# Kernel tuning notes

Hardware: AMD Instinct MI355X
Metric: run time of the kernel (lower is better)

The kernel has to match this reference:

```python
import jax, jax.numpy as jnp
import numpy as np
import math

HIDDEN = 1024
HEADS = 16
HEAD = HIDDEN // HEADS
B, N = 2, 2048
NEG_INF = -10000.0


def setup_inputs() -> dict:
    key = jax.random.key(0)
    k1, k2, k3, k4, k5 = jax.random.split(key, 5)
    s = 1.0 / math.sqrt(HIDDEN)
    return {
        "encodings": jax.random.normal(k1, (B, N, HIDDEN), dtype=jnp.float32),
        "attn_w": jax.random.uniform(k2, (3 * HIDDEN, HIDDEN), minval=-s, maxval=s, dtype=jnp.float32),
        "attn_b": jax.random.uniform(k3, (3 * HIDDEN,), minval=-s, maxval=s, dtype=jnp.float32),
        "out_w": jax.random.uniform(k4, (HIDDEN, HIDDEN), minval=-s, maxval=s, dtype=jnp.float32),
        "out_b": jax.random.uniform(k5, (HIDDEN,), minval=-s, maxval=s, dtype=jnp.float32),
    }


def reference(encodings, attn_w, attn_b, out_w, out_b):
    b, n, _ = encodings.shape
    qkv = encodings @ attn_w.T + attn_b                      # [b, n, 3*hidden]
    # 'b n (h l) -> b h n l' with l = 3*head_size
    qkv = qkv.reshape(b, n, HEADS, 3 * HEAD).transpose(0, 2, 1, 3)  # [b, h, n, 3d]
    q, k, v = jnp.split(qkv, 3, axis=-1)                     # each [b, h, n, d]
    # causal mask: key index k attends only if k <= q
    mask = jnp.arange(n)[:, None] <= jnp.arange(n)[None, :]  # [k, q]
    scores = jnp.einsum('bhki,bhqi->bhkq', k, q) / math.sqrt(HEAD)
    scores = jnp.where(mask, scores, NEG_INF)
    probs = jax.nn.softmax(scores, axis=2)                   # softmax over k
    combined = jnp.einsum('bhkq,bhkl->bhql', probs, v)       # [b, h, n, d]
    out = combined.transpose(0, 2, 1, 3).reshape(b, n, HIDDEN)
    return out @ out_w.T + out_b
```

## Files before the change

### kernel.cpp

```cpp
#include <hip/hip_runtime.h>
#include <hip/hip_bf16.h>
#include <stdint.h>

#define HIDDEN 1024
#define NHEADS 16
#define DHEAD  64
#define BATCH  2
#define SEQ    2048
#define MROWS  (BATCH*SEQ)
#define QKVC   (3*HIDDEN)

typedef unsigned short u16;
typedef unsigned int   u32;
typedef __bf16 bf16x8 __attribute__((ext_vector_type(8)));
typedef __bf16 bf16x2 __attribute__((ext_vector_type(2)));
typedef float  f32x4  __attribute__((ext_vector_type(4)));
typedef float  f32x16 __attribute__((ext_vector_type(16)));
typedef short  s16x4  __attribute__((ext_vector_type(4)));
typedef u16    u16x8  __attribute__((ext_vector_type(8)));
typedef u32    u32x2  __attribute__((ext_vector_type(2)));

typedef const __attribute__((address_space(1))) void gvoid_t;
typedef       __attribute__((address_space(3))) void lvoid_t;

__device__ __forceinline__ gvoid_t* to_glob(const void* p){
  return (gvoid_t*)(uintptr_t)p;
}
__device__ __forceinline__ lvoid_t* to_lds(void* p){
  return (lvoid_t*)(uintptr_t)p;
}
__device__ __forceinline__ u32 lds_off(const void* p){
  return (u32)(uintptr_t)p;
}

__device__ __forceinline__ u16 f2bf(float x){
  __bf16 h = (__bf16)x;
  return __builtin_bit_cast(u16, h);
}
__device__ __forceinline__ u32 pk2(float a, float b){
  bf16x2 t = { (__bf16)a, (__bf16)b };
  return __builtin_bit_cast(u32, t);
}

#define MFMA32(a, b, c) __builtin_amdgcn_mfma_f32_32x32x16_bf16(a, b, c, 0, 0, 0)

__global__ __launch_bounds__(256) void k_cvt(const float* __restrict__ in,
                                             u16* __restrict__ out, int n4){
  int i = blockIdx.x * 256 + threadIdx.x;
  if (i >= n4) return;
  const float4 v = reinterpret_cast<const float4*>(in)[i];
  ushort4 o;
  o.x = f2bf(v.x); o.y = f2bf(v.y); o.z = f2bf(v.z); o.w = f2bf(v.w);
  reinterpret_cast<ushort4*>(out)[i] = o;
}

template<int NC, bool BF16OUT>
__global__ __launch_bounds__(256) void k_gemm(const u16* __restrict__ A,
                                              const u16* __restrict__ B,
                                              const float* __restrict__ bias,
                                              void* __restrict__ C){
  constexpr int K = HIDDEN;
  __shared__ u16 As[2][128*32];
  __shared__ u16 Bs[2][128*32];
  const int m0 = blockIdx.x * 128;
  const int n0 = blockIdx.y * 128;
  const int tid = threadIdx.x;
  const int w = tid >> 6, l = tid & 63;
  const int wr = w >> 1, wc = w & 1;

  const f32x4 fz = {0.f, 0.f, 0.f, 0.f};
  f32x4 acc[4][4];
  #pragma unroll
  for (int i = 0; i < 4; ++i)
    #pragma unroll
    for (int j = 0; j < 4; ++j) acc[i][j] = fz;

  const u16* ap = A + (size_t)(m0 + (tid >> 2)) * K + (tid & 3) * 8;
  const u16* bp = B + (size_t)(n0 + (tid >> 2)) * K + (tid & 3) * 8;

  auto stage = [&](int k0, int buf){
    __builtin_amdgcn_global_load_lds(to_glob(ap + k0),        to_lds(&As[buf][w*512]),        16, 0, 0);
    __builtin_amdgcn_global_load_lds(to_glob(ap + 64*K + k0), to_lds(&As[buf][2048 + w*512]), 16, 0, 0);
    __builtin_amdgcn_global_load_lds(to_glob(bp + k0),        to_lds(&Bs[buf][w*512]),        16, 0, 0);
    __builtin_amdgcn_global_load_lds(to_glob(bp + 64*K + k0), to_lds(&Bs[buf][2048 + w*512]), 16, 0, 0);
  };

  stage(0, 0);
  __syncthreads();

  for (int k0 = 0; k0 < K; k0 += 32){
    const int cur = (k0 >> 5) & 1;
    if (k0 + 32 < K) stage(k0 + 32, cur ^ 1);

    bf16x8 af[4], bfr[4];
    #pragma unroll
    for (int mf = 0; mf < 4; ++mf)
      af[mf]  = *(const bf16x8*)&As[cur][(wr*64 + mf*16 + (l & 15))*32 + (l >> 4)*8];
    #pragma unroll
    for (int nf = 0; nf < 4; ++nf)
      bfr[nf] = *(const bf16x8*)&Bs[cur][(wc*64 + nf*16 + (l & 15))*32 + (l >> 4)*8];
    #pragma unroll
    for (int mf = 0; mf < 4; ++mf)
      #pragma unroll
      for (int nf = 0; nf < 4; ++nf)
        acc[mf][nf] = __builtin_amdgcn_mfma_f32_16x16x32_bf16(af[mf], bfr[nf], acc[mf][nf], 0, 0, 0);

    __syncthreads();
  }

  #pragma unroll
  for (int nf = 0; nf < 4; ++nf){
    const int col = n0 + wc*64 + nf*16 + (l & 15);
    const float bv = bias[col];
    #pragma unroll
    for (int mf = 0; mf < 4; ++mf){
      #pragma unroll
      for (int r = 0; r < 4; ++r){
        const int row = m0 + wr*64 + mf*16 + (l >> 4)*4 + r;
        const float v = acc[mf][nf][r] + bv;
        if constexpr (BF16OUT) ((u16*)C)[(size_t)row * NC + col] = f2bf(v);
        else                   ((float*)C)[(size_t)row * NC + col] = v;
      }
    }
  }
}

__global__ __launch_bounds__(256, 4) void k_attn(const u16* __restrict__ qkv,
                                                 u16* __restrict__ aout){
  __shared__ u16 smem[16384];

  const int bh = blockIdx.x;
  const int b  = bh >> 4;
  const int h  = bh & 15;
  const int qt = 31 - blockIdx.y;
  const int tid = threadIdx.x;
  const int l  = tid & 63;
  const int w  = tid >> 6;
  const int hr = w >> 1;
  const int wr = w & 1;
  const int t128 = tid & 127;
  const int lw = t128 >> 6;
  const int U  = qt + 1;
  const int kb = hr ? U : 0;
  const int q0 = qt*64 + wr*32;
  const size_t base = (size_t)b * SEQ * QKVC + (size_t)h * 192;
  const float CEXP = 0.18033688011112042f;

  u16* const Kreg = smem + hr*8192;
  u16* const Vreg = smem + hr*8192 + 4096;

  const int cgK = (t128 & 7) ^ ((t128 >> 3) & 7);
  const u16* const baseK = qkv + base + (size_t)(t128 >> 3) * QKVC + 64 + cgK * 8;
  const int vk = ((t128 >> 5) << 2) | ((t128 >> 1) & 3);
  const int vd = (((t128 >> 3) & 3) << 4) | ((t128 & 1) << 3);
  const u16* const baseV = qkv + base + (size_t)vk * QKVC + 128 + vd;

  auto stage = [&](int u, int cb){
    const u16* pk = baseK + (size_t)u * 32 * QKVC;
    const u16* pv = baseV + (size_t)u * 32 * QKVC;
    #pragma unroll
    for (int t = 0; t < 2; ++t){
      __builtin_amdgcn_global_load_lds(to_glob(pk + t*16*QKVC),
                                       to_lds(&Kreg[cb*2048 + t*1024 + lw*512]), 16, 0, 0);
      __builtin_amdgcn_global_load_lds(to_glob(pv + t*16*QKVC),
                                       to_lds(&Vreg[cb*2048 + t*1024 + lw*512]), 16, 0, 0);
    }
  };

  bf16x8 qf[4];
  {
    const u16* qp = qkv + base + (size_t)(q0 + (l & 31)) * QKVC + (l >> 5) * 8;
    #pragma unroll
    for (int dd = 0; dd < 4; ++dd) qf[dd] = *(const bf16x8*)(qp + dd*16);
  }

  f32x16 o0{}, o1{};
  float m = -1e30f, lsum = 0.f;

  stage(kb, 0);
  __syncthreads();

  const u32 vbase = lds_off(Vreg) + (l & 15)*8 + ((l >> 4) & 1)*128 + (l >> 5)*1024;

  for (int it = 0; it < U; ++it){
    const int cur = it & 1;
    const int u = kb + it;
    if (it + 1 < U) stage(kb + it + 1, cur ^ 1);

    f32x16 a0{};
    const int r0 = l & 31;
    #pragma unroll
    for (int dd = 0; dd < 4; ++dd){
      const int c = dd*2 + (l >> 5);
      const bf16x8 k0 = *(const bf16x8*)&Kreg[cur*2048 + r0*64 + ((c ^ (r0 & 7)))*8];
      a0 = MFMA32(k0, qf[dd], a0);
    }

    if (u*32 + 31 > q0){
      const int qg = q0 + (l & 31);
      #pragma unroll
      for (int r = 0; r < 16; ++r){
        const int kg = u*32 + (r & 3) + 8*(r >> 2) + 4*(l >> 5);
        if (kg > qg) a0[r] = -1e30f;
      }
    }

    float pm = -1e30f;
    #pragma unroll
    for (int r = 0; r < 16; ++r) pm = fmaxf(pm, a0[r]);
    pm = fmaxf(pm, __shfl(pm, l ^ 32));

    s16x4 tr[8];
    {
      const u32 vb = vbase + (cur ? 4096u : 0u);
      #pragma unroll
      for (int kk = 0; kk < 2; ++kk){
        asm volatile("ds_read_b64_tr_b16 %0, %4 offset:0\n\t"
                     "ds_read_b64_tr_b16 %1, %4 offset:512\n\t"
                     "ds_read_b64_tr_b16 %2, %4 offset:256\n\t"
                     "ds_read_b64_tr_b16 %3, %4 offset:768"
                     : "=&v"(tr[kk*4+0]), "=&v"(tr[kk*4+1]),
                       "=&v"(tr[kk*4+2]), "=&v"(tr[kk*4+3])
                     : "v"(vb + kk*2048));
      }
    }

    if (__any(pm > m + 64.f)){
      const float mn = fmaxf(m, pm);
      const float corr = exp2f((m - mn) * CEXP);
      m = mn;
      lsum *= corr;
      #pragma unroll
      for (int r = 0; r < 16; ++r){
        const int row = (r & 3) + 8*(r >> 2) + 4*(l >> 5);
        const float cr = __shfl(corr, row | (l & 32));
        o0[r] *= cr; o1[r] *= cr;
      }
    }
    #pragma unroll
    for (int r = 0; r < 16; ++r){
      const float p = exp2f((a0[r] - m) * CEXP);
      lsum += p;
      a0[r] = p;
    }

    asm volatile("s_waitcnt lgkmcnt(0)" ::: "memory");
    __builtin_amdgcn_sched_barrier(0);
    #pragma unroll
    for (int kk = 0; kk < 2; ++kk){
      const int o = kk * 8;
      const u32 x0 = pk2(a0[o+0], a0[o+1]);
      const u32 x1 = pk2(a0[o+2], a0[o+3]);
      const u32 y0 = pk2(a0[o+4], a0[o+5]);
      const u32 y1 = pk2(a0[o+6], a0[o+7]);
      const u32x2 r0v = __builtin_amdgcn_permlane32_swap(x0, y0, false, false);
      const u32x2 r1v = __builtin_amdgcn_permlane32_swap(x1, y1, false, false);
      union { u32 wd[4]; bf16x8 v; } af;
      af.wd[0] = r0v[0]; af.wd[1] = r1v[0]; af.wd[2] = r0v[1]; af.wd[3] = r1v[1];
      union { s16x4 hh[2]; bf16x8 v; } b0, b1;
      b0.hh[0] = tr[kk*4+0]; b0.hh[1] = tr[kk*4+1];
      b1.hh[0] = tr[kk*4+2]; b1.hh[1] = tr[kk*4+3];
      o0 = MFMA32(af.v, b0.v, o0);
      o1 = MFMA32(af.v, b1.v, o1);
    }

    __syncthreads();
  }

  lsum += __shfl(lsum, l ^ 32);
  float* const Osh  = (float*)smem;
  float2* const MLsh = (float2*)((char*)smem + 16384);

  if (hr == 1){
    #pragma unroll
    for (int r = 0; r < 16; ++r){
      Osh[wr*2048 + l*32 + r]      = o0[r];
      Osh[wr*2048 + l*32 + 16 + r] = o1[r];
    }
    MLsh[wr*64 + l] = float2{m, lsum};
  }
  __syncthreads();

  if (hr == 0){
    const float2 ml1 = MLsh[wr*64 + l];
    const float mm = fmaxf(m, ml1.x);
    const float c0 = exp2f((m - mm) * CEXP);
    const float c1 = exp2f((ml1.x - mm) * CEXP);
    const float lm = lsum*c0 + ml1.y*c1;
    const float a0q = c0 / lm;
    const float a1q = c1 / lm;
    #pragma unroll
    for (int r = 0; r < 16; ++r){
      const int row = (r & 3) + 8*(r >> 2) + 4*(l >> 5);
      const float f0 = __shfl(a0q, row | (l & 32));
      const float f1 = __shfl(a1q, row | (l & 32));
      const int qg = q0 + row;
      u16* op = aout + (size_t)(b*SEQ + qg) * HIDDEN + h*64 + (l & 31);
      op[0]  = f2bf(o0[r]*f0 + Osh[wr*2048 + l*32 + r]*f1);
      op[32] = f2bf(o1[r]*f0 + Osh[wr*2048 + l*32 + 16 + r]*f1);
    }
  }
}

extern "C" void kernel_launch(void* const* d_in, const int* in_sizes, int n_in,
                              void* d_out, int out_size, void* d_ws, size_t ws_size,
                              hipStream_t stream){
  const float* enc    = (const float*)d_in[0];
  const float* attn_w = (const float*)d_in[1];
  const float* attn_b = (const float*)d_in[2];
  const float* out_w  = (const float*)d_in[3];
  const float* out_b  = (const float*)d_in[4];

  char* ws = (char*)d_ws;
  u16* enc_bf = (u16*)(ws);
  u16* wa_bf  = (u16*)(ws + (size_t)( 8u << 20));
  u16* wo_bf  = (u16*)(ws + (size_t)(14u << 20));
  u16* qkv    = (u16*)(ws + (size_t)(16u << 20));
  u16* aout   = enc_bf;

  k_cvt<<<dim3((MROWS*HIDDEN/4 + 255)/256), 256, 0, stream>>>(enc,    enc_bf, MROWS*HIDDEN/4);
  k_cvt<<<dim3((QKVC*HIDDEN/4  + 255)/256), 256, 0, stream>>>(attn_w, wa_bf,  QKVC*HIDDEN/4);
  k_cvt<<<dim3((HIDDEN*HIDDEN/4+ 255)/256), 256, 0, stream>>>(out_w,  wo_bf,  HIDDEN*HIDDEN/4);

  k_gemm<QKVC,  true ><<<dim3(MROWS/128, QKVC/128),  256, 0, stream>>>(enc_bf, wa_bf, attn_b, qkv);
  k_attn<<<dim3(32, 32), 256, 0, stream>>>(qkv, aout);
  k_gemm<HIDDEN, false><<<dim3(MROWS/128, HIDDEN/128), 256, 0, stream>>>(aout, wo_bf, out_b, d_out);
}
```

Measured before the change: 111.1 us.

## Fuse conversion kernels and restructure attention to two waves sharing K/V per tile

Merges the three fp32-to-bf16 conversion launches into one kernel that dispatches on index range, which removes launch overhead. The attention block shrinks from four waves to two. Each wave now handles both 32-row query halves of a 64-row tile, so every K tile read from LDS feeds two MFMAs and the per-iteration block barrier goes away in favour of per-wave vmcnt waits on its own staged buffers. This doubles accumulator register pressure per wave and lowers occupancy hints, trading thread-level parallelism for data reuse and less synchronisation.

After: 141.9 us. 27.8% more time.

```diff
diff --git a/kernel.cpp b/kernel.cpp
--- a/kernel.cpp
+++ b/kernel.cpp
@@ -44,14 +44,25 @@
 
 #define MFMA32(a, b, c) __builtin_amdgcn_mfma_f32_32x32x16_bf16(a, b, c, 0, 0, 0)
 
-__global__ __launch_bounds__(256) void k_cvt(const float* __restrict__ in,
-                                             u16* __restrict__ out, int n4){
+#define CVT_N0 1048576
+#define CVT_N1  786432
+#define CVT_N2  262144
+__global__ __launch_bounds__(256) void k_cvt3(const float* __restrict__ e,
+                                              const float* __restrict__ wa,
+                                              const float* __restrict__ wo,
+                                              u16* __restrict__ eb,
+                                              u16* __restrict__ wab,
+                                              u16* __restrict__ wob){
   int i = blockIdx.x * 256 + threadIdx.x;
-  if (i >= n4) return;
-  const float4 v = reinterpret_cast<const float4*>(in)[i];
+  const float* src; u16* dst;
+  if (i < CVT_N0){ src = e; dst = eb; }
+  else if (i < CVT_N0 + CVT_N1){ i -= CVT_N0; src = wa; dst = wab; }
+  else if (i < CVT_N0 + CVT_N1 + CVT_N2){ i -= CVT_N0 + CVT_N1; src = wo; dst = wob; }
+  else return;
+  const float4 v = reinterpret_cast<const float4*>(src)[i];
   ushort4 o;
   o.x = f2bf(v.x); o.y = f2bf(v.y); o.z = f2bf(v.z); o.w = f2bf(v.w);
-  reinterpret_cast<ushort4*>(out)[i] = o;
+  reinterpret_cast<ushort4*>(dst)[i] = o;
 }
 
 template<int NC, bool BF16OUT>
@@ -125,94 +136,113 @@
   }
 }
 
-__global__ __launch_bounds__(256, 4) void k_attn(const u16* __restrict__ qkv,
+__global__ __launch_bounds__(128, 3) void k_attn(const u16* __restrict__ qkv,
                                                  u16* __restrict__ aout){
   __shared__ u16 smem[16384];
 
   const int bh = blockIdx.x;
   const int b  = bh >> 4;
   const int h  = bh & 15;
-  const int qt = 31 - blockIdx.y;
+  const int g  = 31 - (int)blockIdx.y;
   const int tid = threadIdx.x;
-  const int l  = tid & 63;
-  const int w  = tid >> 6;
-  const int hr = w >> 1;
-  const int wr = w & 1;
-  const int t128 = tid & 127;
-  const int lw = t128 >> 6;
-  const int U  = qt + 1;
-  const int kb = hr ? U : 0;
-  const int q0 = qt*64 + wr*32;
+  const int w = tid >> 6;
+  const int l = tid & 63;
+  const int U  = g + 1;
+  const int kb = w ? U : 0;
+  const int q0lo = g*64, q0hi = g*64 + 32;
   const size_t base = (size_t)b * SEQ * QKVC + (size_t)h * 192;
   const float CEXP = 0.18033688011112042f;
 
-  u16* const Kreg = smem + hr*8192;
-  u16* const Vreg = smem + hr*8192 + 4096;
-
-  const int cgK = (t128 & 7) ^ ((t128 >> 3) & 7);
-  const u16* const baseK = qkv + base + (size_t)(t128 >> 3) * QKVC + 64 + cgK * 8;
-  const int vk = ((t128 >> 5) << 2) | ((t128 >> 1) & 3);
-  const int vd = (((t128 >> 3) & 3) << 4) | ((t128 & 1) << 3);
+  u16* const Kw = smem + w*8192;
+  u16* const Vw = smem + w*8192 + 4096;
+
+  const int cgK = (l & 7) ^ ((l >> 3) & 7);
+  const u16* const baseK = qkv + base + (size_t)(l >> 3) * QKVC + 64 + cgK*8;
+  const int vk = ((l >> 5) << 2) | ((l >> 1) & 3);
+  const int vd = (((l >> 3) & 3) << 4) | ((l & 1) << 3);
   const u16* const baseV = qkv + base + (size_t)vk * QKVC + 128 + vd;
 
   auto stage = [&](int u, int cb){
     const u16* pk = baseK + (size_t)u * 32 * QKVC;
     const u16* pv = baseV + (size_t)u * 32 * QKVC;
     #pragma unroll
-    for (int t = 0; t < 2; ++t){
-      __builtin_amdgcn_global_load_lds(to_glob(pk + t*16*QKVC),
-                                       to_lds(&Kreg[cb*2048 + t*1024 + lw*512]), 16, 0, 0);
-      __builtin_amdgcn_global_load_lds(to_glob(pv + t*16*QKVC),
-                                       to_lds(&Vreg[cb*2048 + t*1024 + lw*512]), 16, 0, 0);
+    for (int t = 0; t < 4; ++t){
+      __builtin_amdgcn_global_load_lds(to_glob(pk + t*8*QKVC), to_lds(&Kw[cb*2048 + t*512]), 16, 0, 0);
+      __builtin_amdgcn_global_load_lds(to_glob(pv + t*8*QKVC), to_lds(&Vw[cb*2048 + t*512]), 16, 0, 0);
     }
   };
 
-  bf16x8 qf[4];
+  bf16x8 qfL[4], qfH[4];
   {
-    const u16* qp = qkv + base + (size_t)(q0 + (l & 31)) * QKVC + (l >> 5) * 8;
-    #pragma unroll
-    for (int dd = 0; dd < 4; ++dd) qf[dd] = *(const bf16x8*)(qp + dd*16);
-  }
-
-  f32x16 o0{}, o1{};
-  float m = -1e30f, lsum = 0.f;
+    const u16* qa = qkv + base + (size_t)(q0lo + (l & 31)) * QKVC + (l >> 5) * 8;
+    const u16* qb = qkv + base + (size_t)(q0hi + (l & 31)) * QKVC + (l >> 5) * 8;
+    #pragma unroll
+    for (int dd = 0; dd < 4; ++dd){
+      qfL[dd] = *(const bf16x8*)(qa + dd*16);
+      qfH[dd] = *(const bf16x8*)(qb + dd*16);
+    }
+  }
+
+  f32x16 oL0{}, oL1{}, oH0{}, oH1{};
+  float mL = -1e30f, lsL = 0.f, mH = -1e30f, lsH = 0.f;
 
   stage(kb, 0);
-  __syncthreads();
-
-  const u32 vbase = lds_off(Vreg) + (l & 15)*8 + ((l >> 4) & 1)*128 + (l >> 5)*1024;
+
+  const u32 vbytes = lds_off(Vw) + (l & 15)*8 + ((l >> 4) & 1)*128 + (l >> 5)*1024;
 
   for (int it = 0; it < U; ++it){
-    const int cur = it & 1;
-    const int u = kb + it;
-    if (it + 1 < U) stage(kb + it + 1, cur ^ 1);
-
-    f32x16 a0{};
+    const int cb = it & 1;
+    const int u  = kb + it;
+
+    if (it + 1 < U){
+      stage(kb + it + 1, cb ^ 1);
+      asm volatile("s_waitcnt vmcnt(8)" ::: "memory");
+    } else {
+      asm volatile("s_waitcnt vmcnt(0)" ::: "memory");
+    }
+    __builtin_amdgcn_sched_barrier(0);
+
+    const bool loAct = (u*32 <= q0lo + 31);
+
+    f32x16 aL{}, aH{};
     const int r0 = l & 31;
     #pragma unroll
     for (int dd = 0; dd < 4; ++dd){
       const int c = dd*2 + (l >> 5);
-      const bf16x8 k0 = *(const bf16x8*)&Kreg[cur*2048 + r0*64 + ((c ^ (r0 & 7)))*8];
-      a0 = MFMA32(k0, qf[dd], a0);
-    }
-
-    if (u*32 + 31 > q0){
-      const int qg = q0 + (l & 31);
+      const bf16x8 kf = *(const bf16x8*)&Kw[cb*2048 + r0*64 + ((c ^ (r0 & 7)))*8];
+      aL = MFMA32(kf, qfL[dd], aL);
+      aH = MFMA32(kf, qfH[dd], aH);
+    }
+
+    if (loAct && u*32 + 31 > q0lo){
+      const int qg = q0lo + (l & 31);
       #pragma unroll
       for (int r = 0; r < 16; ++r){
         const int kg = u*32 + (r & 3) + 8*(r >> 2) + 4*(l >> 5);
-        if (kg > qg) a0[r] = -1e30f;
-      }
-    }
-
-    float pm = -1e30f;
-    #pragma unroll
-    for (int r = 0; r < 16; ++r) pm = fmaxf(pm, a0[r]);
-    pm = fmaxf(pm, __shfl(pm, l ^ 32));
+        if (kg > qg) aL[r] = -1e30f;
+      }
+    }
+    if (u*32 + 31 > q0hi){
+      const int qg = q0hi + (l & 31);
+      #pragma unroll
+      for (int r = 0; r < 16; ++r){
+        const int kg = u*32 + (r & 3) + 8*(r >> 2) + 4*(l >> 5);
+        if (kg > qg) aH[r] = -1e30f;
+      }
+    }
+
+    float pmL = -1e30f, pmH = -1e30f;
+    #pragma unroll
+    for (int r = 0; r < 16; ++r){
+      pmL = fmaxf(pmL, aL[r]);
+      pmH = fmaxf(pmH, aH[r]);
+    }
+    pmL = fmaxf(pmL, __shfl(pmL, l ^ 32));
+    pmH = fmaxf(pmH, __shfl(pmH, l ^ 32));
 
     s16x4 tr[8];
     {
-      const u32 vb = vbase + (cur ? 4096u : 0u);
+      const u32 vb = vbytes + (cb ? 4096u : 0u);
       #pragma unroll
       for (int kk = 0; kk < 2; ++kk){
         asm volatile("ds_read_b64_tr_b16 %0, %4 offset:0\n\t"
@@ -225,79 +255,128 @@
       }
     }
 
-    if (__any(pm > m + 64.f)){
-      const float mn = fmaxf(m, pm);
-      const float corr = exp2f((m - mn) * CEXP);
-      m = mn;
-      lsum *= corr;
-      #pragma unroll
-      for (int r = 0; r < 16; ++r){
-        const int row = (r & 3) + 8*(r >> 2) + 4*(l >> 5);
-        const float cr = __shfl(corr, row | (l & 32));
-        o0[r] *= cr; o1[r] *= cr;
-      }
-    }
-    #pragma unroll
-    for (int r = 0; r < 16; ++r){
-      const float p = exp2f((a0[r] - m) * CEXP);
-      lsum += p;
-      a0[r] = p;
+    if (loAct){
+      if (__any(pmL > mL + 64.f)){
+        const float mn = fmaxf(mL, pmL);
+        const float corr = exp2f((mL - mn) * CEXP);
+        mL = mn; lsL *= corr;
+        #pragma unroll
+        for (int r = 0; r < 16; ++r){
+          const int row = (r & 3) + 8*(r >> 2) + 4*(l >> 5);
+          const float cr = __shfl(corr, row | (l & 32));
+          oL0[r] *= cr; oL1[r] *= cr;
+        }
+      }
+      #pragma unroll
+      for (int r = 0; r < 16; ++r){
+        const float p = exp2f((aL[r] - mL) * CEXP);
+        lsL += p; aL[r] = p;
+      }
+    }
+    {
+      if (__any(pmH > mH + 64.f)){
+        const float mn = fmaxf(mH, pmH);
+        const float corr = exp2f((mH - mn) * CEXP);
+        mH = mn; lsH *= corr;
+        #pragma unroll
+        for (int r = 0; r < 16; ++r){
+          const int row = (r & 3) + 8*(r >> 2) + 4*(l >> 5);
+          const float cr = __shfl(corr, row | (l & 32));
+          oH0[r] *= cr; oH1[r] *= cr;
+        }
+      }
+      #pragma unroll
+      for (int r = 0; r < 16; ++r){
+        const float p = exp2f((aH[r] - mH) * CEXP);
+        lsH += p; aH[r] = p;
+      }
     }
 
     asm volatile("s_waitcnt lgkmcnt(0)" ::: "memory");
     __builtin_amdgcn_sched_barrier(0);
     #pragma unroll
     for (int kk = 0; kk < 2; ++kk){
-      const int o = kk * 8;
-      const u32 x0 = pk2(a0[o+0], a0[o+1]);
-      const u32 x1 = pk2(a0[o+2], a0[o+3]);
-      const u32 y0 = pk2(a0[o+4], a0[o+5]);
-      const u32 y1 = pk2(a0[o+6], a0[o+7]);
-      const u32x2 r0v = __builtin_amdgcn_permlane32_swap(x0, y0, false, false);
-      const u32x2 r1v = __builtin_amdgcn_permlane32_swap(x1, y1, false, false);
-      union { u32 wd[4]; bf16x8 v; } af;
-      af.wd[0] = r0v[0]; af.wd[1] = r1v[0]; af.wd[2] = r0v[1]; af.wd[3] = r1v[1];
       union { s16x4 hh[2]; bf16x8 v; } b0, b1;
       b0.hh[0] = tr[kk*4+0]; b0.hh[1] = tr[kk*4+1];
       b1.hh[0] = tr[kk*4+2]; b1.hh[1] = tr[kk*4+3];
-      o0 = MFMA32(af.v, b0.v, o0);
-      o1 = MFMA32(af.v, b1.v, o1);
-    }
-
-    __syncthreads();
-  }
-
-  lsum += __shfl(lsum, l ^ 32);
-  float* const Osh  = (float*)smem;
-  float2* const MLsh = (float2*)((char*)smem + 16384);
-
-  if (hr == 1){
+      const int o = kk * 8;
+      if (loAct){
+        const u32 x0 = pk2(aL[o+0], aL[o+1]);
+        const u32 x1 = pk2(aL[o+2], aL[o+3]);
+        const u32 y0 = pk2(aL[o+4], aL[o+5]);
+        const u32 y1 = pk2(aL[o+6], aL[o+7]);
+        const u32x2 r0v = __builtin_amdgcn_permlane32_swap(x0, y0, false, false);
+        const u32x2 r1v = __builtin_amdgcn_permlane32_swap(x1, y1, false, false);
+        union { u32 wd[4]; bf16x8 v; } af;
+        af.wd[0] = r0v[0]; af.wd[1] = r1v[0]; af.wd[2] = r0v[1]; af.wd[3] = r1v[1];
+        oL0 = MFMA32(af.v, b0.v, oL0);
+        oL1 = MFMA32(af.v, b1.v, oL1);
+      }
+      {
+        const u32 x0 = pk2(aH[o+0], aH[o+1]);
+        const u32 x1 = pk2(aH[o+2], aH[o+3]);
+        const u32 y0 = pk2(aH[o+4], aH[o+5]);
+        const u32 y1 = pk2(aH[o+6], aH[o+7]);
+        const u32x2 r0v = __builtin_amdgcn_permlane32_swap(x0, y0, false, false);
+        const u32x2 r1v = __builtin_amdgcn_permlane32_swap(x1, y1, false, false);
+        union { u32 wd[4]; bf16x8 v; } af;
+        af.wd[0] = r0v[0]; af.wd[1] = r1v[0]; af.wd[2] = r0v[1]; af.wd[3] = r1v[1];
+        oH0 = MFMA32(af.v, b0.v, oH0);
+        oH1 = MFMA32(af.v, b1.v, oH1);
+      }
+    }
+  }
+
+  lsL += __shfl(lsL, l ^ 32);
+  lsH += __shfl(lsH, l ^ 32);
+  __syncthreads();
+  float*  const O1 = (float*)(smem + 8192);
+  float4* const ML = (float4*)smem;
+  if (w == 1){
     #pragma unroll
     for (int r = 0; r < 16; ++r){
-      Osh[wr*2048 + l*32 + r]      = o0[r];
-      Osh[wr*2048 + l*32 + 16 + r] = o1[r];
-    }
-    MLsh[wr*64 + l] = float2{m, lsum};
+      O1[0*1024 + l*16 + r] = oL0[r];
+      O1[1*1024 + l*16 + r] = oL1[r];
+      O1[2*1024 + l*16 + r] = oH0[r];
+      O1[3*1024 + l*16 + r] = oH1[r];
+    }
+    ML[l] = float4{mL, lsL, mH, lsH};
   }
   __syncthreads();
 
-  if (hr == 0){
-    const float2 ml1 = MLsh[wr*64 + l];
-    const float mm = fmaxf(m, ml1.x);
-    const float c0 = exp2f((m - mm) * CEXP);
-    const float c1 = exp2f((ml1.x - mm) * CEXP);
-    const float lm = lsum*c0 + ml1.y*c1;
-    const float a0q = c0 / lm;
-    const float a1q = c1 / lm;
-    #pragma unroll
-    for (int r = 0; r < 16; ++r){
-      const int row = (r & 3) + 8*(r >> 2) + 4*(l >> 5);
-      const float f0 = __shfl(a0q, row | (l & 32));
-      const float f1 = __shfl(a1q, row | (l & 32));
-      const int qg = q0 + row;
-      u16* op = aout + (size_t)(b*SEQ + qg) * HIDDEN + h*64 + (l & 31);
-      op[0]  = f2bf(o0[r]*f0 + Osh[wr*2048 + l*32 + r]*f1);
-      op[32] = f2bf(o1[r]*f0 + Osh[wr*2048 + l*32 + 16 + r]*f1);
+  if (w == 0){
+    const float4 ml1 = ML[l];
+    {
+      const float mm = fmaxf(mL, ml1.x);
+      const float c0 = exp2f((mL - mm) * CEXP);
+      const float c1 = exp2f((ml1.x - mm) * CEXP);
+      const float lm = lsL*c0 + ml1.y*c1;
+      const float a0q = c0 / lm, a1q = c1 / lm;
+      #pragma unroll
+      for (int r = 0; r < 16; ++r){
+        const int row = (r & 3) + 8*(r >> 2) + 4*(l >> 5);
+        const float f0 = __shfl(a0q, row | (l & 32));
+        const float f1 = __shfl(a1q, row | (l & 32));
+        u16* op = aout + (size_t)(b*SEQ + q0lo + row) * HIDDEN + h*64 + (l & 31);
+        op[0]  = f2bf(oL0[r]*f0 + O1[0*1024 + l*16 + r]*f1);
+        op[32] = f2bf(oL1[r]*f0 + O1[1*1024 + l*16 + r]*f1);
+      }
+    }
+    {
+      const float mm = fmaxf(mH, ml1.z);
+      const float c0 = exp2f((mH - mm) * CEXP);
+      const float c1 = exp2f((ml1.z - mm) * CEXP);
+      const float lm = lsH*c0 + ml1.w*c1;
+      const float a0q = c0 / lm, a1q = c1 / lm;
+      #pragma unroll
+      for (int r = 0; r < 16; ++r){
+        const int row = (r & 3) + 8*(r >> 2) + 4*(l >> 5);
+        const float f0 = __shfl(a0q, row | (l & 32));
+        const float f1 = __shfl(a1q, row | (l & 32));
+        u16* op = aout + (size_t)(b*SEQ + q0hi + row) * HIDDEN + h*64 + (l & 31);
+        op[0]  = f2bf(oH0[r]*f0 + O1[2*1024 + l*16 + r]*f1);
+        op[32] = f2bf(oH1[r]*f0 + O1[3*1024 + l*16 + r]*f1);
+      }
     }
   }
 }
@@ -318,11 +397,10 @@
   u16* qkv    = (u16*)(ws + (size_t)(16u << 20));
   u16* aout   = enc_bf;
 
-  k_cvt<<<dim3((MROWS*HIDDEN/4 + 255)/256), 256, 0, stream>>>(enc,    enc_bf, MROWS*HIDDEN/4);
-  k_cvt<<<dim3((QKVC*HIDDEN/4  + 255)/256), 256, 0, stream>>>(attn_w, wa_bf,  QKVC*HIDDEN/4);
-  k_cvt<<<dim3((HIDDEN*HIDDEN/4+ 255)/256), 256, 0, stream>>>(out_w,  wo_bf,  HIDDEN*HIDDEN/4);
+  k_cvt3<<<dim3((CVT_N0+CVT_N1+CVT_N2 + 255)/256), 256, 0, stream>>>(
+      enc, attn_w, out_w, enc_bf, wa_bf, wo_bf);
 
   k_gemm<QKVC,  true ><<<dim3(MROWS/128, QKVC/128),  256, 0, stream>>>(enc_bf, wa_bf, attn_b, qkv);
-  k_attn<<<dim3(32, 32), 256, 0, stream>>>(qkv, aout);
+  k_attn<<<dim3(32, 32), 128, 0, stream>>>(qkv, aout);
   k_gemm<HIDDEN, false><<<dim3(MROWS/128, HIDDEN/128), 256, 0, stream>>>(aout, wo_bf, out_b, d_out);
 }
```

## Triple-buffer K/V in attention with vmcnt waits and merge conversion kernels

Applied to the files above, without the earlier changes.

The attention kernel's K/V staging goes from double to triple buffering with a prefetch distance of two tiles. The per-iteration __syncthreads is replaced by an s_waitcnt vmcnt plus a raw s_barrier, which aims to hide global-to-LDS load latency. The three fp32-to-bf16 conversion launches are merged into one kernel to save launch overhead. LDS use per block grows to 48KB, which may reduce occupancy. The vmcnt(4) count and the duplicate stage when U==1 need to be correct for every case.

Result: slower. 117.1 us (+5.4%).

```diff
diff --git a/kernel.cpp b/kernel.cpp
--- a/kernel.cpp
+++ b/kernel.cpp
@@ -44,14 +44,25 @@
 
 #define MFMA32(a, b, c) __builtin_amdgcn_mfma_f32_32x32x16_bf16(a, b, c, 0, 0, 0)
 
-__global__ __launch_bounds__(256) void k_cvt(const float* __restrict__ in,
-                                             u16* __restrict__ out, int n4){
+#define CVT_N0 1048576
+#define CVT_N1  786432
+#define CVT_N2  262144
+__global__ __launch_bounds__(256) void k_cvt3(const float* __restrict__ e,
+                                              const float* __restrict__ wa,
+                                              const float* __restrict__ wo,
+                                              u16* __restrict__ eb,
+                                              u16* __restrict__ wab,
+                                              u16* __restrict__ wob){
   int i = blockIdx.x * 256 + threadIdx.x;
-  if (i >= n4) return;
-  const float4 v = reinterpret_cast<const float4*>(in)[i];
+  const float* src; u16* dst;
+  if (i < CVT_N0){ src = e; dst = eb; }
+  else if (i < CVT_N0 + CVT_N1){ i -= CVT_N0; src = wa; dst = wab; }
+  else if (i < CVT_N0 + CVT_N1 + CVT_N2){ i -= CVT_N0 + CVT_N1; src = wo; dst = wob; }
+  else return;
+  const float4 v = reinterpret_cast<const float4*>(src)[i];
   ushort4 o;
   o.x = f2bf(v.x); o.y = f2bf(v.y); o.z = f2bf(v.z); o.w = f2bf(v.w);
-  reinterpret_cast<ushort4*>(out)[i] = o;
+  reinterpret_cast<ushort4*>(dst)[i] = o;
 }
 
 template<int NC, bool BF16OUT>
@@ -127,7 +138,7 @@
 
 __global__ __launch_bounds__(256, 4) void k_attn(const u16* __restrict__ qkv,
                                                  u16* __restrict__ aout){
-  __shared__ u16 smem[16384];
+  __shared__ u16 smem[24576];
 
   const int bh = blockIdx.x;
   const int b  = bh >> 4;
@@ -146,8 +157,8 @@
   const size_t base = (size_t)b * SEQ * QKVC + (size_t)h * 192;
   const float CEXP = 0.18033688011112042f;
 
-  u16* const Kreg = smem + hr*8192;
-  u16* const Vreg = smem + hr*8192 + 4096;
+  u16* const Kreg = smem + hr*12288;
+  u16* const Vreg = smem + hr*12288 + 6144;
 
   const int cgK = (t128 & 7) ^ ((t128 >> 3) & 7);
   const u16* const baseK = qkv + base + (size_t)(t128 >> 3) * QKVC + 64 + cgK * 8;
@@ -178,21 +189,27 @@
   float m = -1e30f, lsum = 0.f;
 
   stage(kb, 0);
-  __syncthreads();
-
-  const u32 vbase = lds_off(Vreg) + (l & 15)*8 + ((l >> 4) & 1)*128 + (l >> 5)*1024;
-
+  stage(kb + (U > 1 ? 1 : 0), 1);
+
+  const u32 vbytes = lds_off(Vreg) + (l & 15)*8 + ((l >> 4) & 1)*128 + (l >> 5)*1024;
+
+  int cb = 0;
   for (int it = 0; it < U; ++it){
-    const int cur = it & 1;
     const int u = kb + it;
-    if (it + 1 < U) stage(kb + it + 1, cur ^ 1);
+
+    asm volatile("s_waitcnt vmcnt(4)" ::: "memory");
+    __builtin_amdgcn_sched_barrier(0);
+    __builtin_amdgcn_s_barrier();
+    __builtin_amdgcn_sched_barrier(0);
+
+    if (it + 2 < U) stage(kb + it + 2, (cb == 0) ? 2 : cb - 1);
 
     f32x16 a0{};
     const int r0 = l & 31;
     #pragma unroll
     for (int dd = 0; dd < 4; ++dd){
       const int c = dd*2 + (l >> 5);
-      const bf16x8 k0 = *(const bf16x8*)&Kreg[cur*2048 + r0*64 + ((c ^ (r0 & 7)))*8];
+      const bf16x8 k0 = *(const bf16x8*)&Kreg[cb*2048 + r0*64 + ((c ^ (r0 & 7)))*8];
       a0 = MFMA32(k0, qf[dd], a0);
     }
 
@@ -212,7 +229,7 @@
 
     s16x4 tr[8];
     {
-      const u32 vb = vbase + (cur ? 4096u : 0u);
+      const u32 vb = vbytes + (u32)cb * 4096u;
       #pragma unroll
       for (int kk = 0; kk < 2; ++kk){
         asm volatile("ds_read_b64_tr_b16 %0, %4 offset:0\n\t"
@@ -264,10 +281,11 @@
       o1 = MFMA32(af.v, b1.v, o1);
     }
 
-    __syncthreads();
+    cb = (cb == 2) ? 0 : cb + 1;
   }
 
   lsum += __shfl(lsum, l ^ 32);
+  __syncthreads();
   float* const Osh  = (float*)smem;
   float2* const MLsh = (float2*)((char*)smem + 16384);
 
@@ -318,9 +336,8 @@
   u16* qkv    = (u16*)(ws + (size_t)(16u << 20));
   u16* aout   = enc_bf;
 
-  k_cvt<<<dim3((MROWS*HIDDEN/4 + 255)/256), 256, 0, stream>>>(enc,    enc_bf, MROWS*HIDDEN/4);
-  k_cvt<<<dim3((QKVC*HIDDEN/4  + 255)/256), 256, 0, stream>>>(attn_w, wa_bf,  QKVC*HIDDEN/4);
-  k_cvt<<<dim3((HIDDEN*HIDDEN/4+ 255)/256), 256, 0, stream>>>(out_w,  wo_bf,  HIDDEN*HIDDEN/4);
+  k_cvt3<<<dim3((CVT_N0+CVT_N1+CVT_N2 + 255)/256), 256, 0, stream>>>(
+      enc, attn_w, out_w, enc_bf, wa_bf, wo_bf);
 
   k_gemm<QKVC,  true ><<<dim3(MROWS/128, QKVC/128),  256, 0, stream>>>(enc_bf, wa_bf, attn_b, qkv);
   k_attn<<<dim3(32, 32), 256, 0, stream>>>(qkv, aout);
```
